# Kernel tuning notes

Hardware: AMD Instinct MI355X
Metric: run time of the kernel (lower is better)

## Reference

```python
import jax, jax.numpy as jnp
import numpy as np

C, L, N, D, V = 8, 4096, 4096, 128, 100000

def setup_inputs() -> dict:
    key = jax.random.key(0)
    k1, k2, k3, k4 = jax.random.split(key, 4)
    ngram_seq = jax.random.randint(k1, (C, N), 0, V, dtype=jnp.int64)
    hidden_state = jax.random.normal(k2, (L, D), dtype=jnp.float32)
    word_ngram_mask_matrix = jax.random.uniform(k3, (C, L, N), dtype=jnp.float32)
    channel_ids = jnp.arange(C, dtype=jnp.int64)
    W_emb = jax.random.normal(k4, (V, D), dtype=jnp.float32)
    W_emb = W_emb.at[0].set(0.0)  # padding_idx=0
    W_channel = jax.random.normal(jax.random.fold_in(key, 5), (C, 1), dtype=jnp.float32)
    return {"ngram_seq": ngram_seq, "hidden_state": hidden_state,
            "word_ngram_mask_matrix": word_ngram_mask_matrix,
            "channel_ids": channel_ids, "W_emb": W_emb, "W_channel": W_channel}

def reference(ngram_seq, hidden_state, word_ngram_mask_matrix, channel_ids, W_emb, W_channel):
    temper = jnp.float32(np.sqrt(D))
    emb = W_emb[ngram_seq]                                   # [C, N, D]
    # u = (emb @ hidden^T)/temper, then permute -> [C, L, N]
    u = jnp.einsum('cnd,ld->cln', emb, hidden_state) / temper
    mask = jnp.clip(word_ngram_mask_matrix, 0.0, 1.0)        # [C, L, N]
    delta_exp_u = jnp.exp(u) * mask                          # masked exp (no max-shift, as in source)
    attention = delta_exp_u / (jnp.sum(delta_exp_u, axis=2, keepdims=True) + 1e-10)
    character_attention = jnp.einsum('cln,cnd->cld', attention, emb)  # [C, L, D]
    channel_w = W_channel[channel_ids]                       # [C, 1]
    channel_w = jax.nn.softmax(channel_w, axis=1)            # trivial over size-1 dim, kept for fidelity
    character_attention = character_attention * channel_w.reshape(-1, 1, 1)
    out = jnp.transpose(character_attention, (1, 0, 2)).reshape(L, C * D)  # [L, C*D]
    return out
```

## Files before the change

kernel.cpp:

```cpp
#include <hip/hip_runtime.h>


typedef __bf16 bf16_t;
typedef bf16_t bf16x8 __attribute__((ext_vector_type(8)));
typedef bf16_t bf16x2 __attribute__((ext_vector_type(2)));
typedef float  f32x16 __attribute__((ext_vector_type(16)));
typedef float  f32x4  __attribute__((ext_vector_type(4)));

#define C_ 8
#define L_ 4096
#define N_ 4096
#define D_ 128

__global__ __launch_bounds__(512, 2) void ngram_attn_kernel(
    const int* __restrict__ seq,
    const float* __restrict__ hidden,
    const float* __restrict__ mask,
    const float* __restrict__ Wemb,
    float* __restrict__ out)
{
  __shared__ bf16_t End[128][136];
  __shared__ bf16_t Et [128][136];
  __shared__ bf16_t Ps [128][136];
  __shared__ float  dpart[2][128];
  __shared__ float  dinv[128];

  const int bid  = blockIdx.x;
  const int c    = bid & 7;
  const int l0   = (bid >> 3) * 128;
  const int tid  = threadIdx.x;
  const int wv   = tid >> 6;
  const int lane = tid & 63;
  const int mrow = lane & 31;
  const int hi   = lane >> 5;
  const int lsl  = wv & 3;
  const int nh   = wv >> 2;

  const float inv_temper = 0.08838834764831845f;
  const int* seq_c = seq + (size_t)c * N_;

  bf16x8 Ha[8];
  {
    const float* hrow = hidden + (size_t)(l0 + lsl * 32 + mrow) * D_ + hi * 8;
    #pragma unroll
    for (int ks = 0; ks < 8; ++ks) {
      f32x4 h0 = *(const f32x4*)(hrow + ks * 16);
      f32x4 h1 = *(const f32x4*)(hrow + ks * 16 + 4);
      Ha[ks] = (bf16x8){ (bf16_t)h0[0], (bf16_t)h0[1], (bf16_t)h0[2], (bf16_t)h0[3],
                         (bf16_t)h1[0], (bf16_t)h1[1], (bf16_t)h1[2], (bf16_t)h1[3] };
    }
  }

  const int lrow_base = lsl * 32 + 4 * hi;
  const int ncol      = nh * 64 + mrow;
  const float* mrow_base = mask + ((size_t)c * L_ + l0 + lrow_base) * N_ + ncol;

  int   sidxB[4];
  f32x4 ereg[8];
  float mreg[32];

  {
    int sidxA[4];
    #pragma unroll
    for (int rep = 0; rep < 2; ++rep) {
      int u = tid + rep * 512, np = u & 63;
      sidxA[2 * rep + 0] = seq_c[2 * np];
      sidxA[2 * rep + 1] = seq_c[2 * np + 1];
    }
    #pragma unroll
    for (int rep = 0; rep < 2; ++rep) {
      int u = tid + rep * 512, g = u >> 6;
      const f32x4* r1 = (const f32x4*)(Wemb + (size_t)sidxA[2 * rep + 0] * D_ + g * 8);
      const f32x4* r2 = (const f32x4*)(Wemb + (size_t)sidxA[2 * rep + 1] * D_ + g * 8);
      ereg[4 * rep + 0] = r1[0]; ereg[4 * rep + 1] = r1[1];
      ereg[4 * rep + 2] = r2[0]; ereg[4 * rep + 3] = r2[1];
    }
    #pragma unroll
    for (int rep = 0; rep < 2; ++rep) {
      int u = tid + rep * 512, np = u & 63;
      sidxB[2 * rep + 0] = seq_c[128 + 2 * np];
      sidxB[2 * rep + 1] = seq_c[128 + 2 * np + 1];
    }
    #pragma unroll
    for (int r = 0; r < 16; ++r) {
      const float* mp = mrow_base + (size_t)((r & 3) + 8 * (r >> 2)) * N_;
      mreg[2 * r + 0] = __builtin_nontemporal_load(mp);
      mreg[2 * r + 1] = __builtin_nontemporal_load(mp + 32);
    }
  }

  f32x16 Oacc0, Oacc1;
  float dacc[16];
  #pragma unroll
  for (int i = 0; i < 16; ++i) { Oacc0[i] = 0.f; Oacc1[i] = 0.f; dacc[i] = 0.f; }

  #pragma unroll 1
  for (int nt = 0; nt < 32; ++nt) {
    __syncthreads();

    #pragma unroll
    for (int rep = 0; rep < 2; ++rep) {
      int u = tid + rep * 512;
      int np = u & 63, g = u >> 6;
      int n1 = 2 * np, n2 = n1 + 1;
      f32x4 a0 = ereg[4 * rep + 0], a1 = ereg[4 * rep + 1];
      f32x4 b0 = ereg[4 * rep + 2], b1 = ereg[4 * rep + 3];
      bf16x8 e1 = { (bf16_t)a0[0], (bf16_t)a0[1], (bf16_t)a0[2], (bf16_t)a0[3],
                    (bf16_t)a1[0], (bf16_t)a1[1], (bf16_t)a1[2], (bf16_t)a1[3] };
      bf16x8 e2 = { (bf16_t)b0[0], (bf16_t)b0[1], (bf16_t)b0[2], (bf16_t)b0[3],
                    (bf16_t)b1[0], (bf16_t)b1[1], (bf16_t)b1[2], (bf16_t)b1[3] };
      *(bf16x8*)&End[n1][g * 8] = e1;
      *(bf16x8*)&End[n2][g * 8] = e2;
      #pragma unroll
      for (int i = 0; i < 8; ++i) {
        bf16x2 t = { e1[i], e2[i] };
        *(bf16x2*)&Et[g * 8 + i][n1] = t;
      }
    }
    __syncthreads();

    f32x16 S0, S1;
    #pragma unroll
    for (int i = 0; i < 16; ++i) { S0[i] = 0.f; S1[i] = 0.f; }
    #pragma unroll
    for (int ks = 0; ks < 8; ++ks) {
      bf16x8 b0 = *(const bf16x8*)&End[nh * 64 + 0  + mrow][ks * 16 + hi * 8];
      bf16x8 b1 = *(const bf16x8*)&End[nh * 64 + 32 + mrow][ks * 16 + hi * 8];
      S0 = __builtin_amdgcn_mfma_f32_32x32x16_bf16(Ha[ks], b0, S0, 0, 0, 0);
      S1 = __builtin_amdgcn_mfma_f32_32x32x16_bf16(Ha[ks], b1, S1, 0, 0, 0);
    }

    {
      int ntp = (nt < 31) ? nt + 1 : 31;
      #pragma unroll
      for (int rep = 0; rep < 2; ++rep) {
        int u = tid + rep * 512, g = u >> 6;
        const f32x4* r1 = (const f32x4*)(Wemb + (size_t)sidxB[2 * rep + 0] * D_ + g * 8);
        const f32x4* r2 = (const f32x4*)(Wemb + (size_t)sidxB[2 * rep + 1] * D_ + g * 8);
        ereg[4 * rep + 0] = r1[0]; ereg[4 * rep + 1] = r1[1];
        ereg[4 * rep + 2] = r2[0]; ereg[4 * rep + 3] = r2[1];
      }
      int nts = (nt < 30) ? nt + 2 : 31;
      const int* sp = seq_c + nts * 128;
      #pragma unroll
      for (int rep = 0; rep < 2; ++rep) {
        int u = tid + rep * 512, np = u & 63;
        sidxB[2 * rep + 0] = sp[2 * np];
        sidxB[2 * rep + 1] = sp[2 * np + 1];
      }
      (void)ntp;
    }

    #pragma unroll
    for (int r = 0; r < 16; ++r) {
      int lr = lsl * 32 + (r & 3) + 8 * (r >> 2) + 4 * hi;
      float m0 = fminf(fmaxf(mreg[2 * r + 0], 0.f), 1.f);
      float m1 = fminf(fmaxf(mreg[2 * r + 1], 0.f), 1.f);
      float w0 = __expf(S0[r] * inv_temper) * m0;
      float w1 = __expf(S1[r] * inv_temper) * m1;
      dacc[r] += w0 + w1;
      Ps[lr][nh * 64 + mrow]      = (bf16_t)w0;
      Ps[lr][nh * 64 + 32 + mrow] = (bf16_t)w1;
    }

    {
      int ntp = (nt < 31) ? nt + 1 : 31;
      const float* mb = mrow_base + (size_t)ntp * 128;
      #pragma unroll
      for (int r = 0; r < 16; ++r) {
        const float* mp = mb + (size_t)((r & 3) + 8 * (r >> 2)) * N_;
        mreg[2 * r + 0] = __builtin_nontemporal_load(mp);
        mreg[2 * r + 1] = __builtin_nontemporal_load(mp + 32);
      }
    }
    __syncthreads();

    #pragma unroll
    for (int ks = 0; ks < 8; ++ks) {
      bf16x8 a  = *(const bf16x8*)&Ps[lsl * 32 + mrow][ks * 16 + hi * 8];
      bf16x8 b0 = *(const bf16x8*)&Et[nh * 64 + 0  + mrow][ks * 16 + hi * 8];
      bf16x8 b1 = *(const bf16x8*)&Et[nh * 64 + 32 + mrow][ks * 16 + hi * 8];
      Oacc0 = __builtin_amdgcn_mfma_f32_32x32x16_bf16(a, b0, Oacc0, 0, 0, 0);
      Oacc1 = __builtin_amdgcn_mfma_f32_32x32x16_bf16(a, b1, Oacc1, 0, 0, 0);
    }
  }

  #pragma unroll
  for (int r = 0; r < 16; ++r) {
    float v = dacc[r];
    v += __shfl_xor(v, 1, 64);
    v += __shfl_xor(v, 2, 64);
    v += __shfl_xor(v, 4, 64);
    v += __shfl_xor(v, 8, 64);
    v += __shfl_xor(v, 16, 64);
    if (mrow == 0)
      dpart[nh][lsl * 32 + (r & 3) + 8 * (r >> 2) + 4 * hi] = v;
  }
  __syncthreads();
  if (tid < 128)
    dinv[tid] = 1.0f / (dpart[0][tid] + dpart[1][tid] + 1e-10f);
  __syncthreads();

  #pragma unroll
  for (int r = 0; r < 16; ++r) {
    int lr = lsl * 32 + (r & 3) + 8 * (r >> 2) + 4 * hi;
    float inv = dinv[lr];
    size_t base = (size_t)(l0 + lr) * (C_ * D_) + c * D_ + nh * 64 + mrow;
    __builtin_nontemporal_store(Oacc0[r] * inv, out + base);
    __builtin_nontemporal_store(Oacc1[r] * inv, out + base + 32);
  }
}

extern "C" void kernel_launch(void* const* d_in, const int* in_sizes, int n_in,
                              void* d_out, int out_size, void* d_ws, size_t ws_size,
                              hipStream_t stream) {
  (void)in_sizes; (void)n_in; (void)out_size; (void)d_ws; (void)ws_size;
  const int*   seq    = (const int*)d_in[0];
  const float* hidden = (const float*)d_in[1];
  const float* mask   = (const float*)d_in[2];
  const float* Wemb   = (const float*)d_in[4];
  float* out = (float*)d_out;
  ngram_attn_kernel<<<dim3(256), dim3(512), 0, stream>>>(seq, hidden, mask, Wemb, out);
}
```

Before: 832.7 us.

## Pre-gather embeddings into bf16 row and transposed workspace via prep kernel

Adds a prep kernel that gathers the embedding rows per channel, converts them to bf16, and writes both row-major and transposed copies to workspace. The main attention kernel then streams these contiguous bf16 tiles with vector loads and stores, replacing the per-tile fp32 gather, conversion and scattered 2-element transposed LDS stores. This removes gather latency and the LDS transpose from the hot loop. The cost is an extra kernel launch plus the workspace write and read traffic, although it is small next to the mask stream.

```diff
diff --git a/kernel.cpp b/kernel.cpp
--- a/kernel.cpp
+++ b/kernel.cpp
@@ -3,7 +3,6 @@
 
 typedef __bf16 bf16_t;
 typedef bf16_t bf16x8 __attribute__((ext_vector_type(8)));
-typedef bf16_t bf16x2 __attribute__((ext_vector_type(2)));
 typedef float  f32x16 __attribute__((ext_vector_type(16)));
 typedef float  f32x4  __attribute__((ext_vector_type(4)));
 
@@ -12,11 +11,56 @@
 #define N_ 4096
 #define D_ 128
 
+__global__ __launch_bounds__(256, 4) void prep_kernel(
+    const int* __restrict__ seq,
+    const float* __restrict__ Wemb,
+    bf16_t* __restrict__ En,
+    bf16_t* __restrict__ Et)
+{
+  __shared__ bf16_t T[128][132];
+
+  const int bid = blockIdx.x;
+  const int c   = bid & 7;
+  const int n0  = (bid >> 3) * 128;
+  const int t   = threadIdx.x;
+
+  {
+    const int row  = t >> 1;
+    const int half = t & 1;
+    const int idx  = seq[c * N_ + n0 + row];
+    const float* src = Wemb + (size_t)idx * D_ + half * 64;
+    bf16_t* dstE = En + ((size_t)c * N_ + n0 + row) * D_ + half * 64;
+    #pragma unroll
+    for (int j = 0; j < 8; ++j) {
+      f32x4 a = *(const f32x4*)(src + j * 8);
+      f32x4 b = *(const f32x4*)(src + j * 8 + 4);
+      bf16x8 e = { (bf16_t)a[0], (bf16_t)a[1], (bf16_t)a[2], (bf16_t)a[3],
+                   (bf16_t)b[0], (bf16_t)b[1], (bf16_t)b[2], (bf16_t)b[3] };
+      *(bf16x8*)&T[row][half * 64 + j * 8] = e;
+      *(bf16x8*)(dstE + j * 8) = e;
+    }
+  }
+  __syncthreads();
+
+  {
+    const int d  = t >> 1;
+    const int nh = t & 1;
+    bf16_t* dstT = Et + ((size_t)c * D_ + d) * N_ + n0 + nh * 64;
+    #pragma unroll
+    for (int j = 0; j < 8; ++j) {
+      bf16x8 e;
+      #pragma unroll
+      for (int i = 0; i < 8; ++i) e[i] = T[nh * 64 + j * 8 + i][d];
+      *(bf16x8*)(dstT + j * 8) = e;
+    }
+  }
+}
+
 __global__ __launch_bounds__(512, 2) void ngram_attn_kernel(
-    const int* __restrict__ seq,
     const float* __restrict__ hidden,
     const float* __restrict__ mask,
-    const float* __restrict__ Wemb,
+    const bf16_t* __restrict__ EnWs,
+    const bf16_t* __restrict__ EtWs,
     float* __restrict__ out)
 {
   __shared__ bf16_t End[128][136];
@@ -29,15 +73,16 @@
   const int c    = bid & 7;
   const int l0   = (bid >> 3) * 128;
   const int tid  = threadIdx.x;
+  const int lane = tid & 63;
   const int wv   = tid >> 6;
-  const int lane = tid & 63;
   const int mrow = lane & 31;
   const int hi   = lane >> 5;
   const int lsl  = wv & 3;
   const int nh   = wv >> 2;
 
   const float inv_temper = 0.08838834764831845f;
-  const int* seq_c = seq + (size_t)c * N_;
+  const bf16_t* en_c = EnWs + (size_t)c * N_ * D_;
+  const bf16_t* et_c = EtWs + (size_t)c * D_ * N_;
 
   bf16x8 Ha[8];
   {
@@ -55,38 +100,20 @@
   const int ncol      = nh * 64 + mrow;
   const float* mrow_base = mask + ((size_t)c * L_ + l0 + lrow_base) * N_ + ncol;
 
-  int   sidxB[4];
-  f32x4 ereg[8];
-  float mreg[32];
-
-  {
-    int sidxA[4];
-    #pragma unroll
-    for (int rep = 0; rep < 2; ++rep) {
-      int u = tid + rep * 512, np = u & 63;
-      sidxA[2 * rep + 0] = seq_c[2 * np];
-      sidxA[2 * rep + 1] = seq_c[2 * np + 1];
-    }
-    #pragma unroll
-    for (int rep = 0; rep < 2; ++rep) {
-      int u = tid + rep * 512, g = u >> 6;
-      const f32x4* r1 = (const f32x4*)(Wemb + (size_t)sidxA[2 * rep + 0] * D_ + g * 8);
-      const f32x4* r2 = (const f32x4*)(Wemb + (size_t)sidxA[2 * rep + 1] * D_ + g * 8);
-      ereg[4 * rep + 0] = r1[0]; ereg[4 * rep + 1] = r1[1];
-      ereg[4 * rep + 2] = r2[0]; ereg[4 * rep + 3] = r2[1];
-    }
-    #pragma unroll
-    for (int rep = 0; rep < 2; ++rep) {
-      int u = tid + rep * 512, np = u & 63;
-      sidxB[2 * rep + 0] = seq_c[128 + 2 * np];
-      sidxB[2 * rep + 1] = seq_c[128 + 2 * np + 1];
-    }
-    #pragma unroll
-    for (int r = 0; r < 16; ++r) {
-      const float* mp = mrow_base + (size_t)((r & 3) + 8 * (r >> 2)) * N_;
-      mreg[2 * r + 0] = __builtin_nontemporal_load(mp);
-      mreg[2 * r + 1] = __builtin_nontemporal_load(mp + 32);
-    }
+  bf16x8 enreg[4], etreg[4];
+  float  mreg[32];
+
+  #pragma unroll
+  for (int r = 0; r < 4; ++r) {
+    int f = r * 512 + tid, rw = f >> 4, cb = (f & 15) * 8;
+    enreg[r] = *(const bf16x8*)(en_c + (size_t)rw * D_ + cb);
+    etreg[r] = *(const bf16x8*)(et_c + (size_t)rw * N_ + cb);
+  }
+  #pragma unroll
+  for (int r = 0; r < 16; ++r) {
+    const float* mp = mrow_base + (size_t)((r & 3) + 8 * (r >> 2)) * N_;
+    mreg[2 * r + 0] = __builtin_nontemporal_load(mp);
+    mreg[2 * r + 1] = __builtin_nontemporal_load(mp + 32);
   }
 
   f32x16 Oacc0, Oacc1;
@@ -99,23 +126,10 @@
     __syncthreads();
 
     #pragma unroll
-    for (int rep = 0; rep < 2; ++rep) {
-      int u = tid + rep * 512;
-      int np = u & 63, g = u >> 6;
-      int n1 = 2 * np, n2 = n1 + 1;
-      f32x4 a0 = ereg[4 * rep + 0], a1 = ereg[4 * rep + 1];
-      f32x4 b0 = ereg[4 * rep + 2], b1 = ereg[4 * rep + 3];
-      bf16x8 e1 = { (bf16_t)a0[0], (bf16_t)a0[1], (bf16_t)a0[2], (bf16_t)a0[3],
-                    (bf16_t)a1[0], (bf16_t)a1[1], (bf16_t)a1[2], (bf16_t)a1[3] };
-      bf16x8 e2 = { (bf16_t)b0[0], (bf16_t)b0[1], (bf16_t)b0[2], (bf16_t)b0[3],
-                    (bf16_t)b1[0], (bf16_t)b1[1], (bf16_t)b1[2], (bf16_t)b1[3] };
-      *(bf16x8*)&End[n1][g * 8] = e1;
-      *(bf16x8*)&End[n2][g * 8] = e2;
-      #pragma unroll
-      for (int i = 0; i < 8; ++i) {
-        bf16x2 t = { e1[i], e2[i] };
-        *(bf16x2*)&Et[g * 8 + i][n1] = t;
-      }
+    for (int r = 0; r < 4; ++r) {
+      int f = r * 512 + tid, rw = f >> 4, cb = (f & 15) * 8;
+      *(bf16x8*)&End[rw][cb] = enreg[r];
+      *(bf16x8*)&Et [rw][cb] = etreg[r];
     }
     __syncthreads();
 
@@ -132,23 +146,14 @@
 
     {
       int ntp = (nt < 31) ? nt + 1 : 31;
+      const bf16_t* enb = en_c + (size_t)ntp * 128 * D_;
+      const bf16_t* etb = et_c + ntp * 128;
       #pragma unroll
-      for (int rep = 0; rep < 2; ++rep) {
-        int u = tid + rep * 512, g = u >> 6;
-        const f32x4* r1 = (const f32x4*)(Wemb + (size_t)sidxB[2 * rep + 0] * D_ + g * 8);
-        const f32x4* r2 = (const f32x4*)(Wemb + (size_t)sidxB[2 * rep + 1] * D_ + g * 8);
-        ereg[4 * rep + 0] = r1[0]; ereg[4 * rep + 1] = r1[1];
-        ereg[4 * rep + 2] = r2[0]; ereg[4 * rep + 3] = r2[1];
+      for (int r = 0; r < 4; ++r) {
+        int f = r * 512 + tid, rw = f >> 4, cb = (f & 15) * 8;
+        enreg[r] = *(const bf16x8*)(enb + (size_t)rw * D_ + cb);
+        etreg[r] = *(const bf16x8*)(etb + (size_t)rw * N_ + cb);
       }
-      int nts = (nt < 30) ? nt + 2 : 31;
-      const int* sp = seq_c + nts * 128;
-      #pragma unroll
-      for (int rep = 0; rep < 2; ++rep) {
-        int u = tid + rep * 512, np = u & 63;
-        sidxB[2 * rep + 0] = sp[2 * np];
-        sidxB[2 * rep + 1] = sp[2 * np + 1];
-      }
-      (void)ntp;
     }
 
     #pragma unroll
@@ -214,11 +219,16 @@
 extern "C" void kernel_launch(void* const* d_in, const int* in_sizes, int n_in,
                               void* d_out, int out_size, void* d_ws, size_t ws_size,
                               hipStream_t stream) {
-  (void)in_sizes; (void)n_in; (void)out_size; (void)d_ws; (void)ws_size;
+  (void)in_sizes; (void)n_in; (void)out_size; (void)ws_size;
   const int*   seq    = (const int*)d_in[0];
   const float* hidden = (const float*)d_in[1];
   const float* mask   = (const float*)d_in[2];
   const float* Wemb   = (const float*)d_in[4];
   float* out = (float*)d_out;
-  ngram_attn_kernel<<<dim3(256), dim3(512), 0, stream>>>(seq, hidden, mask, Wemb, out);
+
+  bf16_t* EnWs = (bf16_t*)d_ws;
+  bf16_t* EtWs = EnWs + (size_t)C_ * N_ * D_;
+
+  prep_kernel<<<dim3(256), dim3(256), 0, stream>>>(seq, Wemb, EnWs, EtWs);
+  ngram_attn_kernel<<<dim3(256), dim3(512), 0, stream>>>(hidden, mask, EnWs, EtWs, out);
 }
```

Result: faster. 746.3 us (-10.4%).
